# Kernel tuning notes

Hardware: AMD Instinct MI355X
Metric: run time of the kernel (lower is better)

The kernel has to match this reference:

```python
import jax, jax.numpy as jnp
import numpy as np

EPS = 1e-5
GRID = 24          # GRID_SIZE
IMG = 96           # IMAGE_SIZE[0]
SCALE = IMG / GRID # 4.0
X0, X1 = -112.0, 224.0
Y0, Y1 = 0.0, 224.0
CIN = 48
CMID = 24
NKP = 4
B = 1024


def _conv(x, w):
    # x: [B,C,H,W], w: [O,I,kh,kw]
    return jax.lax.conv_general_dilated(x, w, (1, 1), 'SAME',
                                        dimension_numbers=('NCHW', 'OIHW', 'NCHW'))


def _head(x, w1, b1, g, be, m, v, w2, b2, sig):
    y = _conv(x, w1) + b1[None, :, None, None]
    inv = jax.lax.rsqrt(v + EPS)
    y = (y - m[None, :, None, None]) * (g * inv)[None, :, None, None] + be[None, :, None, None]
    y = jax.nn.relu(y)
    y = _conv(y, w2) + b2[None, :, None, None]
    return jax.nn.sigmoid(y) if sig else y


def _head_params(key, cout):
    ks = jax.random.split(key, 4)
    w1 = jax.random.normal(ks[0], (CMID, CIN, 3, 3), jnp.float32) * 0.05
    b1 = jnp.zeros((CMID,), jnp.float32)
    g = jnp.ones((CMID,), jnp.float32)
    be = jnp.zeros((CMID,), jnp.float32)
    m = jax.random.normal(ks[1], (CMID,), jnp.float32) * 0.1
    v = jax.random.uniform(ks[2], (CMID,), jnp.float32, 0.5, 1.5)
    w2 = jax.random.normal(ks[3], (cout, CMID, 1, 1), jnp.float32) * 0.05
    b2 = jnp.zeros((cout,), jnp.float32)
    return w1, b1, g, be, m, v, w2, b2


def setup_inputs() -> dict:
    key = jax.random.key(0)
    k0, kc, kk, kr, ko = jax.random.split(key, 5)
    d = {'features': jax.random.normal(k0, (B, CIN * GRID * GRID), jnp.float32)}
    for pref, kk_, cout in (('c', kc, 1), ('k', kk, NKP), ('r', kr, 2 * NKP), ('o', ko, 2 * NKP)):
        w1, b1, g, be, m, v, w2, b2 = _head_params(kk_, cout)
        d[pref + 'w1'], d[pref + 'b1'] = w1, b1
        d[pref + 'g'], d[pref + 'be'] = g, be
        d[pref + 'm'], d[pref + 'v'] = m, v
        d[pref + 'w2'], d[pref + 'b2'] = w2, b2
    return d


def reference(features,
              cw1, cb1, cg, cbe, cm, cv, cw2, cb2,
              kw1, kb1, kg, kbe, km, kv, kw2, kb2,
              rw1, rb1, rg, rbe, rm, rv, rw2, rb2,
              ow1, ob1, og, obe, om, ov, ow2, ob2):
    Bn = features.shape[0]
    x = features.reshape(Bn, CIN, GRID, GRID)
    center = _head(x, cw1, cb1, cg, cbe, cm, cv, cw2, cb2, True)    # [B,1,H,W]
    kp = _head(x, kw1, kb1, kg, kbe, km, kv, kw2, kb2, True)        # [B,N,H,W]
    reg = _head(x, rw1, rb1, rg, rbe, rm, rv, rw2, rb2, False)      # [B,2N,H,W]
    off = _head(x, ow1, ob1, og, obe, om, ov, ow2, ob2, False)      # [B,2N,H,W]

    H = W = GRID
    hm = kp.reshape(Bn, NKP, H * W)
    idx = jnp.argmax(hm, axis=2)                                   # [B,N]
    my = (idx // W).astype(jnp.float32)
    mx = (idx % W).astype(jnp.float32)
    # offset channels: (n*2) -> x, (n*2+1) -> y
    off_r = off.reshape(Bn, NKP, 2, H * W)
    g = jnp.take_along_axis(off_r, idx[:, :, None, None], axis=3)[..., 0]  # [B,N,2]
    ox, oy = g[..., 0], g[..., 1]
    fx = (mx + ox) * SCALE + X0
    fy = (my + oy) * SCALE + Y0
    pix = jnp.stack([fx, fy], axis=-1).reshape(Bn, 2 * NKP)        # [B,8]
    norm = jnp.stack([(fx - X0) / (X1 - X0), (fy - Y0) / (Y1 - Y0)], axis=-1).reshape(Bn, 2 * NKP)
    return (center, kp, reg, off, norm, pix)
```

## Files before the change

kernel.cpp:

```cpp
#include <hip/hip_runtime.h>
#include <stdint.h>

#define HW    576
#define CIN   48
#define NB    1024

#define O_CENTER 0L
#define O_KP     589824L
#define O_REG    2949120L
#define O_OFF    7667712L
#define O_NORM   12386304L
#define O_PIX    12394496L

#define WS_A1    0
#define WS_W2A   82944
#define WS_B1A   89088
#define WS_B2A   89472
#define WS_WKPT  89600
#define WS_B1KP  131072
#define WS_W2KP  131168
#define WS_B2KP  131552
#define WS_WOFFT 131584
#define WS_B1OFF 173056
#define WS_W2OFF 173152
#define WS_B2OFF 174688

typedef short bf16x8 __attribute__((ext_vector_type(8)));
typedef float f32x16 __attribute__((ext_vector_type(16)));

union U4B  { uint4 q; bf16x8 v; };
union U16Q { uint16_t u[8]; uint4 q; };
union U4Q  { uint16_t u[4]; uint2 q; };

__device__ __forceinline__ bf16x8 as_bf(uint4 q){ U4B u; u.q = q; return u.v; }
__device__ __forceinline__ uint16_t f2b(float f){
  union { float f; uint32_t i; } x; x.f = f;
  uint32_t r = x.i + 0x7FFFu + ((x.i >> 16) & 1u);
  return (uint16_t)(r >> 16);
}

struct P32 {
  const float* w1[4]; const float* b1[4]; const float* g[4]; const float* be[4];
  const float* m[4];  const float* v[4];  const float* w2[4]; const float* b2[4];
};

__device__ __forceinline__ void oc_decode(int oc, int& h, int& ch){
  if (oc == 0){ h = 0; ch = 0; }
  else if (oc < 5){ h = 1; ch = oc - 1; }
  else if (oc < 13){ h = 2; ch = oc - 5; }
  else { h = 3; ch = oc - 13; }
}

__global__ void prep_kernel(P32 P, char* __restrict__ wsb){
  const int tid = threadIdx.x;
  __shared__ float sc[96], bfold[96];
  if (tid < 96){
    int h = tid / 24, o = tid % 24;
    float s = P.g[h][o] / sqrtf(P.v[h][o] + 1e-5f);
    sc[tid] = s;
    bfold[tid] = (P.b1[h][o] - P.m[h][o]) * s + P.be[h][o];
  }
  __syncthreads();
  uint16_t* A1 = (uint16_t*)(wsb + WS_A1);
  for (int t = tid; t < 41472; t += 256){
    int j = t & 7, slot = t >> 3;
    int row = slot % 96, sk = slot / 96;
    int g = sk & 1, k3 = (sk >> 1) % 3, sh = (sk >> 1) / 3;
    int ci = k3*16 + g*8 + j;
    int h = row / 24, o = row % 24;
    A1[t] = f2b(P.w1[h][(o*CIN + ci)*9 + sh] * sc[row]);
  }
  uint16_t* W2A = (uint16_t*)(wsb + WS_W2A);
  for (int t = tid; t < 3072; t += 256){
    int j = t & 7, slot = t >> 3;
    int oc = slot & 31, kg = slot >> 5;
    int k = kg*8 + j;
    float val = 0.f;
    if (oc < 21){
      int h, ch; oc_decode(oc, h, ch);
      int hk = k / 24, o = k % 24;
      if (hk == h) val = P.w2[h][ch*24 + o];
    }
    W2A[t] = f2b(val);
  }
  float* B1A = (float*)(wsb + WS_B1A);
  if (tid < 96) B1A[tid] = bfold[tid];
  float* B2A = (float*)(wsb + WS_B2A);
  if (tid < 32){
    float v = 0.f;
    if (tid < 21){ int h, ch; oc_decode(tid, h, ch); v = P.b2[h][ch]; }
    B2A[tid] = v;
  }
  float* WKPT = (float*)(wsb + WS_WKPT);
  for (int t = tid; t < 10368; t += 256){
    int o = t % 24, k = (t/24) % 9, ci = t / 216;
    WKPT[t] = P.w1[1][(o*CIN + ci)*9 + k] * sc[24 + o];
  }
  if (tid < 24) ((float*)(wsb + WS_B1KP))[tid] = bfold[24 + tid];
  if (tid < 96) ((float*)(wsb + WS_W2KP))[tid] = P.w2[1][tid];
  if (tid < 4)  ((float*)(wsb + WS_B2KP))[tid] = P.b2[1][tid];
  float* WOFFT = (float*)(wsb + WS_WOFFT);
  for (int t = tid; t < 10368; t += 256){
    int o = t % 24, k = (t/24) % 9, ci = t / 216;
    WOFFT[t] = P.w1[3][(o*CIN + ci)*9 + k] * sc[72 + o];
  }
  if (tid < 24)  ((float*)(wsb + WS_B1OFF))[tid] = bfold[72 + tid];
  for (int t = tid; t < 384; t += 256) ((float*)(wsb + WS_W2OFF))[t] = P.w2[3][t];
  if (tid < 16)  ((float*)(wsb + WS_B2OFF))[tid] = P.b2[3][tid];
}

__global__ __launch_bounds__(576) void conv_main(
    const float* __restrict__ feat, const char* __restrict__ wsb,
    float* __restrict__ out)
{
  __shared__ __align__(16) char smem[60000];
  const int b = blockIdx.x, tid = threadIdx.x;
  const int wave = tid >> 6, lane = tid & 63;
  const int q = lane >> 5, l31 = lane & 31;

  if (tid < 294){
    int cib = tid / 49, r = tid % 49;
    int slot = cib*625 + ((r < 25) ? r : (r - 24)*25);
    *(uint4*)(smem + slot*16) = make_uint4(0,0,0,0);
  }
  {
    const float* fb = feat + (size_t)b * (CIN*HW);
    int p = tid, py = p / 24, px = p % 24;
    int sbase = (py+1)*25 + (px+1);
    for (int cib = 0; cib < 6; ++cib){
      U16Q t8;
      #pragma unroll
      for (int j = 0; j < 8; ++j) t8.u[j] = f2b(fb[(cib*8 + j)*HW + p]);
      *(uint4*)(smem + (cib*625 + sbase)*16) = t8.q;
    }
  }
  __syncthreads();

  f32x16 acc[3][2] = {};
  const int p0 = wave*64 + l31, p1 = p0 + 32;
  const int py0 = p0/24, px0 = p0%24, py1 = p1/24, px1 = p1%24;
  const uint4* A1 = (const uint4*)(wsb + WS_A1);
  const uint4 zz = make_uint4(0,0,0,0);

  for (int sh = 0; sh < 9; ++sh){
    const int ky = sh / 3, kx = sh % 3;
    const int yb0 = py0 + ky, xb0 = px0 + kx;
    const int yb1 = py1 + ky, xb1 = px1 + kx;
    const bool v0 = (yb0 < 25) && (xb0 < 25);
    const bool v1 = (yb1 < 25) && (xb1 < 25);
    const int so0 = yb0*25 + xb0, so1 = yb1*25 + xb1;
    #pragma unroll
    for (int k3 = 0; k3 < 3; ++k3){
      const int cib = k3*2 + q;
      uint4 r0 = *(const uint4*)(smem + (cib*625 + (v0 ? so0 : 0))*16);
      uint4 r1 = *(const uint4*)(smem + (cib*625 + (v1 ? so1 : 0))*16);
      r0 = v0 ? r0 : zz;
      r1 = v1 ? r1 : zz;
      const bf16x8 bf0 = as_bf(r0), bf1 = as_bf(r1);
      const int abase = ((sh*3 + k3)*2 + q)*96 + l31;
      #pragma unroll
      for (int mt = 0; mt < 3; ++mt){
        const bf16x8 af = as_bf(A1[abase + mt*32]);
        acc[mt][0] = __builtin_amdgcn_mfma_f32_32x32x16_bf16(af, bf0, acc[mt][0], 0, 0, 0);
        acc[mt][1] = __builtin_amdgcn_mfma_f32_32x32x16_bf16(af, bf1, acc[mt][1], 0, 0, 0);
      }
    }
  }
  __syncthreads();

  const float* B1A = (const float*)(wsb + WS_B1A);
  const float* B2A = (const float*)(wsb + WS_B2A);
  const uint4* W2A = (const uint4*)(wsb + WS_W2A);
  char* ybuf = smem + wave*6144;

  #pragma unroll
  for (int st2 = 0; st2 < 2; ++st2){
    const int p = st2 ? p1 : p0;
    #pragma unroll
    for (int mt = 0; mt < 3; ++mt){
      #pragma unroll
      for (int rg = 0; rg < 4; ++rg){
        const int chanbase = mt*32 + rg*8 + q*4;
        const float* bp = B1A + chanbase;
        U4Q t4;
        #pragma unroll
        for (int r0 = 0; r0 < 4; ++r0){
          float y = acc[mt][st2][rg*4 + r0] + bp[r0];
          t4.u[r0] = f2b(fmaxf(y, 0.f));
        }
        *(uint2*)(ybuf + ((mt*4 + rg)*32 + l31)*16 + q*8) = t4.q;
      }
    }
    f32x16 c2 = {};
    #pragma unroll
    for (int k6 = 0; k6 < 6; ++k6){
      const bf16x8 yf = as_bf(*(const uint4*)(ybuf + ((k6*2 + q)*32 + l31)*16));
      const bf16x8 wf = as_bf(W2A[(k6*2 + q)*32 + l31]);
      c2 = __builtin_amdgcn_mfma_f32_32x32x16_bf16(wf, yf, c2, 0, 0, 0);
    }
    #pragma unroll
    for (int r = 0; r < 16; ++r){
      const int oc = (r & 3) + 8*(r >> 2) + 4*q;
      if (oc < 21){
        float v = c2[r] + B2A[oc];
        long base; int sig;
        if (oc == 0){ base = O_CENTER + (long)b*HW; sig = 1; }
        else if (oc < 5){ base = O_KP + ((long)b*4 + (oc-1))*HW; sig = 1; }
        else if (oc < 13){ base = O_REG + ((long)b*8 + (oc-5))*HW; sig = 0; }
        else { base = O_OFF + ((long)b*8 + (oc-13))*HW; sig = 0; }
        out[base + p] = sig ? (1.f / (1.f + __expf(-v))) : v;
      }
    }
  }
}

__global__ __launch_bounds__(576) void kp_select(
    const float* __restrict__ feat, const char* __restrict__ wsb,
    float* __restrict__ out)
{
  __shared__ float simg[8*26*24];
  __shared__ float wk_lds[8*9*24];
  __shared__ float wo_lds[8*9*24];
  __shared__ float ykp [96*24];
  __shared__ float yoff[96*24];
  __shared__ float ywin[4*24];
  __shared__ int   jobL[4*HW];
  __shared__ int   KtotL;
  __shared__ unsigned long long bestL[4];

  const int b = blockIdx.x, tid = threadIdx.x;
  if (tid == 0) KtotL = 0;
  if (tid < 4) bestL[tid] = 0ULL;
  __syncthreads();

  if (tid < 256){
    const int n = tid >> 6, ln = tid & 63;
    const float* sp = out + O_KP + ((long)b*4 + n)*HW;
    float s[9];
    #pragma unroll
    for (int j = 0; j < 9; ++j) s[j] = sp[j*64 + ln];
    float mx = s[0];
    #pragma unroll
    for (int j = 1; j < 9; ++j) mx = fmaxf(mx, s[j]);
    #pragma unroll
    for (int off = 32; off >= 1; off >>= 1)
      mx = fmaxf(mx, __shfl_xor(mx, off, 64));
    const float sm = fminf(mx, 0.999999f);
    const float thr = sm / (sm + (1.f - sm) * 1.1331485f);
    #pragma unroll
    for (int j = 0; j < 9; ++j){
      if (s[j] >= thr){
        const int slot = atomicAdd(&KtotL, 1);
        jobL[slot] = (n << 16) | (j*64 + ln);
      }
    }
  }
  __syncthreads();
  const int Ktot = KtotL;

  const int s24 = tid / 24, omid = tid - s24*24;
  const int dst = (s24 + 1)*24 + omid;
  const float* fb = feat + (size_t)b * (CIN*HW);
  const float* WKPT  = (const float*)(wsb + WS_WKPT);
  const float* WOFFT = (const float*)(wsb + WS_WOFFT);
  const float b1k = ((const float*)(wsb + WS_B1KP))[omid];
  const float b1o = ((const float*)(wsb + WS_B1OFF))[omid];

  for (int g0 = 0; g0 < Ktot; g0 += 96){
    const int Kg = min(96, Ktot - g0);

    int pyc[4], pxc[4];
    #pragma unroll
    for (int c = 0; c < 4; ++c){
      int p = 0;
      if (c*24 + s24 < Kg) p = jobL[g0 + c*24 + s24] & 0xFFFF;
      pyc[c] = p / 24; pxc[c] = p - (p/24)*24;
    }

    float acck[4] = {0.f,0.f,0.f,0.f}, acco[4] = {0.f,0.f,0.f,0.f};

    for (int pass = 0; pass < 6; ++pass){
      __syncthreads();
      if (tid < 384){
        int c = tid / 48, r = tid - c*48;
        int row = (r < 24) ? 0 : 25;
        int col = (r < 24) ? r : r - 24;
        simg[c*624 + row*24 + col] = 0.f;
      }
      #pragma unroll
      for (int c = 0; c < 8; ++c)
        simg[c*624 + dst] = fb[(pass*8 + c)*HW + tid];
      #pragma unroll
      for (int j = 0; j < 3; ++j){
        wk_lds[tid + j*576] = WKPT [pass*1728 + tid + j*576];
        wo_lds[tid + j*576] = WOFFT[pass*1728 + tid + j*576];
      }
      __syncthreads();

      for (int c8 = 0; c8 < 8; ++c8){
        float pch[4][9];
        #pragma unroll
        for (int c = 0; c < 4; ++c) if (c*24 < Kg){
          const int a = c8*624 + pyc[c]*24 + pxc[c];
          const bool wl = (pxc[c] > 0), wr = (pxc[c] < 23);
          #pragma unroll
          for (int dr = 0; dr < 3; ++dr){
            const int aa = a + dr*24;
            pch[c][dr*3+0] = wl ? simg[aa-1] : 0.f;
            pch[c][dr*3+1] = simg[aa];
            pch[c][dr*3+2] = wr ? simg[aa+1] : 0.f;
          }
        }
        const float* wkb = wk_lds + c8*216 + omid;
        const float* wob = wo_lds + c8*216 + omid;
        #pragma unroll
        for (int k = 0; k < 9; ++k){
          const float wk = wkb[k*24];
          const float wo = wob[k*24];
          #pragma unroll
          for (int c = 0; c < 4; ++c) if (c*24 < Kg){
            acck[c] = fmaf(pch[c][k], wk, acck[c]);
            acco[c] = fmaf(pch[c][k], wo, acco[c]);
          }
        }
      }
    }

    #pragma unroll
    for (int c = 0; c < 4; ++c) if (c*24 < Kg){
      const int sl = c*24 + s24;
      ykp [sl*24 + omid] = fmaxf(acck[c] + b1k, 0.f);
      yoff[sl*24 + omid] = fmaxf(acco[c] + b1o, 0.f);
    }
    __syncthreads();

    if (tid < Kg){
      const int cand = g0 + tid;
      const int job = jobL[cand];
      const int n = job >> 16, p = job & 0xFFFF;
      const float* W2KP = (const float*)(wsb + WS_W2KP);
      float v = ((const float*)(wsb + WS_B2KP))[n];
      #pragma unroll
      for (int o = 0; o < 24; ++o)
        v = fmaf(ykp[tid*24 + o], W2KP[n*24 + o], v);
      union { float f; uint32_t u; } cv; cv.f = v;
      const uint32_t key = cv.u ^ (uint32_t)(((int32_t)cv.u >> 31) | (int32_t)0x80000000);
      const unsigned long long pk = ((unsigned long long)key << 32)
                                  | ((unsigned long long)(unsigned)(1023 - p) << 12)
                                  | (unsigned)cand;
      atomicMax(&bestL[n], pk);
    }
    __syncthreads();

    if (tid < 96){
      const int n = tid / 24, o = tid - n*24;
      const int cw = (int)(bestL[n] & 0xFFFu);
      if (cw >= g0 && cw < g0 + Kg)
        ywin[n*24 + o] = yoff[(cw - g0)*24 + o];
    }
    __syncthreads();
  }

  if (tid < 4){
    const int n = tid;
    const unsigned long long bw = bestL[n];
    const int p = 1023 - (int)((bw >> 12) & 0x3FFu);
    const int py = p / 24, px = p % 24;
    const float* W2OFF = (const float*)(wsb + WS_W2OFF);
    const float* B2OFF = (const float*)(wsb + WS_B2OFF);
    float ox = B2OFF[2*n], oy = B2OFF[2*n + 1];
    #pragma unroll
    for (int o = 0; o < 24; ++o){
      const float ym = ywin[n*24 + o];
      ox = fmaf(ym, W2OFF[(2*n)*24 + o], ox);
      oy = fmaf(ym, W2OFF[(2*n + 1)*24 + o], oy);
    }
    const float fx = ((float)px + ox) * 4.f - 112.f;
    const float fy = ((float)py + oy) * 4.f;
    out[O_NORM + b*8 + 2*n    ] = (fx + 112.f) * (1.f/336.f);
    out[O_NORM + b*8 + 2*n + 1] = fy * (1.f/224.f);
    out[O_PIX  + b*8 + 2*n    ] = fx;
    out[O_PIX  + b*8 + 2*n + 1] = fy;
  }
}

extern "C" void kernel_launch(void* const* d_in, const int* in_sizes, int n_in,
                              void* d_out, int out_size, void* d_ws, size_t ws_size,
                              hipStream_t stream)
{
  const float* feat = (const float*)d_in[0];
  P32 P;
  for (int h = 0; h < 4; ++h){
    const int base = 1 + h*8;
    P.w1[h] = (const float*)d_in[base+0];
    P.b1[h] = (const float*)d_in[base+1];
    P.g[h]  = (const float*)d_in[base+2];
    P.be[h] = (const float*)d_in[base+3];
    P.m[h]  = (const float*)d_in[base+4];
    P.v[h]  = (const float*)d_in[base+5];
    P.w2[h] = (const float*)d_in[base+6];
    P.b2[h] = (const float*)d_in[base+7];
  }
  char* wsb = (char*)d_ws;
  float* out = (float*)d_out;

  prep_kernel<<<dim3(1),   256, 0, stream>>>(P, wsb);
  conv_main  <<<dim3(NB),  576, 0, stream>>>(feat, wsb, out);
  kp_select  <<<dim3(NB),  576, 0, stream>>>(feat, wsb, out);
}
```

Baseline: 682.8 us.

## Compute offset-head mid features only at winning argmax positions

The kp_select kernel previously evaluated the offset head's 3x3 conv for every candidate position alongside the keypoint head. Now it computes only the keypoint conv per candidate, picks the argmax, then gathers a 48x3x3 input patch at each of the four winners and evaluates the offset mid layer once per winner with a dot product against weights in the original OIHW layout. This halves the candidate conv FMAs and weight staging, adding a small serial tail that reads features from global memory again. The tie-break key drops the candidate index in favour of the position alone.

```diff
diff --git a/kernel.cpp b/kernel.cpp
--- a/kernel.cpp
+++ b/kernel.cpp
@@ -101,8 +101,8 @@
   if (tid < 4)  ((float*)(wsb + WS_B2KP))[tid] = P.b2[1][tid];
   float* WOFFT = (float*)(wsb + WS_WOFFT);
   for (int t = tid; t < 10368; t += 256){
-    int o = t % 24, k = (t/24) % 9, ci = t / 216;
-    WOFFT[t] = P.w1[3][(o*CIN + ci)*9 + k] * sc[72 + o];
+    int o = t / 432;
+    WOFFT[t] = P.w1[3][t] * sc[72 + o];
   }
   if (tid < 24)  ((float*)(wsb + WS_B1OFF))[tid] = bfold[72 + tid];
   for (int t = tid; t < 384; t += 256) ((float*)(wsb + WS_W2OFF))[t] = P.w2[3][t];
@@ -218,12 +218,11 @@
     const float* __restrict__ feat, const char* __restrict__ wsb,
     float* __restrict__ out)
 {
-  __shared__ float simg[8*26*24];
+  __shared__ __align__(16) float simg[8*26*24];
   __shared__ float wk_lds[8*9*24];
-  __shared__ float wo_lds[8*9*24];
   __shared__ float ykp [96*24];
-  __shared__ float yoff[96*24];
-  __shared__ float ywin[4*24];
+  __shared__ __align__(16) float opatch[4][432];
+  __shared__ float ymidL[4*24];
   __shared__ int   jobL[4*HW];
   __shared__ int   KtotL;
   __shared__ unsigned long long bestL[4];
@@ -261,10 +260,8 @@
   const int s24 = tid / 24, omid = tid - s24*24;
   const int dst = (s24 + 1)*24 + omid;
   const float* fb = feat + (size_t)b * (CIN*HW);
-  const float* WKPT  = (const float*)(wsb + WS_WKPT);
-  const float* WOFFT = (const float*)(wsb + WS_WOFFT);
+  const float* WKPT = (const float*)(wsb + WS_WKPT);
   const float b1k = ((const float*)(wsb + WS_B1KP))[omid];
-  const float b1o = ((const float*)(wsb + WS_B1OFF))[omid];
 
   for (int g0 = 0; g0 < Ktot; g0 += 96){
     const int Kg = min(96, Ktot - g0);
@@ -277,7 +274,7 @@
       pyc[c] = p / 24; pxc[c] = p - (p/24)*24;
     }
 
-    float acck[4] = {0.f,0.f,0.f,0.f}, acco[4] = {0.f,0.f,0.f,0.f};
+    float acck[4] = {0.f,0.f,0.f,0.f};
 
     for (int pass = 0; pass < 6; ++pass){
       __syncthreads();
@@ -291,10 +288,8 @@
       for (int c = 0; c < 8; ++c)
         simg[c*624 + dst] = fb[(pass*8 + c)*HW + tid];
       #pragma unroll
-      for (int j = 0; j < 3; ++j){
-        wk_lds[tid + j*576] = WKPT [pass*1728 + tid + j*576];
-        wo_lds[tid + j*576] = WOFFT[pass*1728 + tid + j*576];
-      }
+      for (int j = 0; j < 3; ++j)
+        wk_lds[tid + j*576] = WKPT[pass*1728 + tid + j*576];
       __syncthreads();
 
       for (int c8 = 0; c8 < 8; ++c8){
@@ -312,16 +307,12 @@
           }
         }
         const float* wkb = wk_lds + c8*216 + omid;
-        const float* wob = wo_lds + c8*216 + omid;
         #pragma unroll
         for (int k = 0; k < 9; ++k){
           const float wk = wkb[k*24];
-          const float wo = wob[k*24];
           #pragma unroll
-          for (int c = 0; c < 4; ++c) if (c*24 < Kg){
+          for (int c = 0; c < 4; ++c) if (c*24 < Kg)
             acck[c] = fmaf(pch[c][k], wk, acck[c]);
-            acco[c] = fmaf(pch[c][k], wo, acco[c]);
-          }
         }
       }
     }
@@ -329,8 +320,7 @@
     #pragma unroll
     for (int c = 0; c < 4; ++c) if (c*24 < Kg){
       const int sl = c*24 + s24;
-      ykp [sl*24 + omid] = fmaxf(acck[c] + b1k, 0.f);
-      yoff[sl*24 + omid] = fmaxf(acco[c] + b1o, 0.f);
+      ykp[sl*24 + omid] = fmaxf(acck[c] + b1k, 0.f);
     }
     __syncthreads();
 
@@ -345,33 +335,56 @@
         v = fmaf(ykp[tid*24 + o], W2KP[n*24 + o], v);
       union { float f; uint32_t u; } cv; cv.f = v;
       const uint32_t key = cv.u ^ (uint32_t)(((int32_t)cv.u >> 31) | (int32_t)0x80000000);
-      const unsigned long long pk = ((unsigned long long)key << 32)
-                                  | ((unsigned long long)(unsigned)(1023 - p) << 12)
-                                  | (unsigned)cand;
+      const unsigned long long pk =
+          ((unsigned long long)key << 32) | (unsigned)(1023 - p);
       atomicMax(&bestL[n], pk);
     }
     __syncthreads();
-
-    if (tid < 96){
-      const int n = tid / 24, o = tid - n*24;
-      const int cw = (int)(bestL[n] & 0xFFFu);
-      if (cw >= g0 && cw < g0 + Kg)
-        ywin[n*24 + o] = yoff[(cw - g0)*24 + o];
-    }
-    __syncthreads();
-  }
+  }
+
+  #pragma unroll
+  for (int j = 0; j < 3; ++j){
+    const int e = tid*3 + j;
+    const int w = e / 432, idx = e - w*432;
+    const int ci = idx / 9, k = idx - ci*9;
+    const int p = 1023 - (int)(bestL[w] & 0xFFFFFFFFu);
+    const int py = p / 24, px = p % 24;
+    const int yy = py + k/3 - 1, xx = px + (k - (k/3)*3) - 1;
+    float v = 0.f;
+    if (yy >= 0 && yy < 24 && xx >= 0 && xx < 24)
+      v = fb[ci*HW + yy*24 + xx];
+    opatch[w][idx] = v;
+  }
+  __syncthreads();
+
+  if (tid < 96){
+    const int n = tid / 24, mid = tid - n*24;
+    const float* wrow = (const float*)(wsb + WS_WOFFT) + mid*432;
+    const float* prow = opatch[n];
+    float s = 0.f;
+    #pragma unroll 4
+    for (int t = 0; t < 108; ++t){
+      const float4 pv = *(const float4*)(prow + t*4);
+      const float4 wv = *(const float4*)(wrow + t*4);
+      s = fmaf(pv.x, wv.x, s);
+      s = fmaf(pv.y, wv.y, s);
+      s = fmaf(pv.z, wv.z, s);
+      s = fmaf(pv.w, wv.w, s);
+    }
+    ymidL[n*24 + mid] = fmaxf(s + ((const float*)(wsb + WS_B1OFF))[mid], 0.f);
+  }
+  __syncthreads();
 
   if (tid < 4){
     const int n = tid;
-    const unsigned long long bw = bestL[n];
-    const int p = 1023 - (int)((bw >> 12) & 0x3FFu);
+    const int p = 1023 - (int)(bestL[n] & 0xFFFFFFFFu);
     const int py = p / 24, px = p % 24;
     const float* W2OFF = (const float*)(wsb + WS_W2OFF);
     const float* B2OFF = (const float*)(wsb + WS_B2OFF);
     float ox = B2OFF[2*n], oy = B2OFF[2*n + 1];
     #pragma unroll
     for (int o = 0; o < 24; ++o){
-      const float ym = ywin[n*24 + o];
+      const float ym = ymidL[n*24 + o];
       ox = fmaf(ym, W2OFF[(2*n)*24 + o], ox);
       oy = fmaf(ym, W2OFF[(2*n + 1)*24 + o], oy);
     }
```

Result: faster. 630.5 us (-7.7%).
